# Performance work log

Measured on AMD Instinct MI355X. Metric: run time of the kernel, lower is better.

The kernel has to match this reference:

```python
import jax, jax.numpy as jnp
import numpy as np

INV_SQRT2 = 0.7071067811865476  # 1/sqrt(2), haar dec filter coefficient


def haar_dwt2(x):
    """Single-level 2D Haar DWT matching pywt.dwt2 (even sizes, so 'symmetric'
    padding never contributes). x: [B, H, W] -> (cA, (cH, cV, cD)),
    each [B, H//2, W//2]. pywt haar: cA=(even+odd)/sqrt2, cD=(even-odd)/sqrt2.
    cH = detail along axis0 / approx along axis1 (pywt 'da')."""
    lo = (x[..., ::2] + x[..., 1::2]) * INV_SQRT2   # approx along cols
    hi = (x[..., ::2] - x[..., 1::2]) * INV_SQRT2   # detail along cols
    cA = (lo[..., ::2, :] + lo[..., 1::2, :]) * INV_SQRT2
    cH = (lo[..., ::2, :] - lo[..., 1::2, :]) * INV_SQRT2
    cV = (hi[..., ::2, :] + hi[..., 1::2, :]) * INV_SQRT2
    cD = (hi[..., ::2, :] - hi[..., 1::2, :]) * INV_SQRT2
    return cA, (cH, cV, cD)


def wavedec2_maps(x, levels):
    """pywt.wavedec2 ordering: [cA_L, (cH_L,cV_L,cD_L), ..., (cH_1,cV_1,cD_1)]."""
    a = x
    details = []
    for _ in range(levels):
        a, d = haar_dwt2(a)
        details.append(d)
    maps = [a]
    for d in reversed(details):
        maps.extend(d)
    return maps  # 1 + 3*levels coefficient maps


def setup_inputs() -> dict:
    key = jax.random.key(0)
    k1, k2 = jax.random.split(key)
    B, H, W_img = 64, 1024, 1024
    x = jax.random.normal(k1, (B, 1, H, W_img), dtype=jnp.float32)
    n_maps = 1 + 3 * 2  # levels=2 -> 7
    W = jax.random.normal(k2, (n_maps, 256), dtype=jnp.float32) * (1.0 / np.sqrt(n_maps))
    b = jnp.zeros((256,), dtype=jnp.float32)
    return {"x": x, "W": W, "b": b}


def reference(x, W, b):
    imgs = x[:, 0]                       # [B, H, W]
    B = imgs.shape[0]
    maps = wavedec2_maps(imgs, 2)        # 7 maps of varying spatial size
    # bilinear resize to 8x8, half-pixel centers == torch align_corners=False
    proc = [jax.image.resize(m, (B, 8, 8), method="bilinear") for m in maps]
    feat = jnp.stack(proc, axis=1)       # [B, 7, 8, 8]
    feat = feat.reshape(B, feat.shape[1], 64).transpose(0, 2, 1)  # [B, 64, 7]
    return feat @ W + b                  # [B, 64, 256]
```

## Files before the change

### kernel.cpp

```cpp
#include <hip/hip_runtime.h>
#include <math.h>

#define IS2 0.70710678118654752440f


__device__ __forceinline__ float tri_f(float x) {
    float a = 1.0f - fabsf(x);
    return a > 0.0f ? a : 0.0f;
}

__global__ void init_weights(float* __restrict__ ws) {
    __shared__ float norm512[8];
    __shared__ float norm256[8];
    int t = threadIdx.x;
    if (t < 8) {
        float c = 64.0f * t + 31.5f;
        float s = 0.0f;
        for (int m = 0; m < 512; ++m) s += tri_f((m - c) * (1.0f / 64.0f));
        norm512[t] = s;
    } else if (t < 16) {
        int i = t - 8;
        float c = 32.0f * i + 15.5f;
        float s = 0.0f;
        for (int m = 0; m < 256; ++m) s += tri_f((m - c) * (1.0f / 32.0f));
        norm256[i] = s;
    }
    __syncthreads();

    float* K2 = ws;
    float* K4 = ws + 4096;
    float* Fc = ws + 6144;

    for (int idx = t; idx < 4096; idx += 256) {
        int m2 = idx >> 3, i = idx & 7;
        K2[idx] = IS2 * tri_f((m2 - (64.0f * i + 31.5f)) * (1.0f / 64.0f)) / norm512[i];
    }
    for (int idx = t; idx < 2048; idx += 256) {
        int m4 = idx >> 3, i = idx & 7;
        K4[idx] = 0.5f * tri_f((m4 - (32.0f * i + 15.5f)) * (1.0f / 32.0f)) / norm256[i];
    }
    for (int idx = t; idx < 32768; idx += 256) {
        int jp = idx >> 10, q = idx & 1023;
        int s = jp >> 3, i = jp & 7;
        float v;
        if (s == 0) {
            v = 0.5f * tri_f(((q >> 2) - (32.0f * i + 15.5f)) * (1.0f / 32.0f)) / norm256[i];
        } else if (s == 1) {
            float sg = ((q & 3) < 2) ? 1.0f : -1.0f;
            v = sg * 0.5f * tri_f(((q >> 2) - (32.0f * i + 15.5f)) * (1.0f / 32.0f)) / norm256[i];
        } else if (s == 2) {
            v = IS2 * tri_f(((q >> 1) - (64.0f * i + 31.5f)) * (1.0f / 64.0f)) / norm512[i];
        } else {
            float sg = ((q & 1) == 0) ? 1.0f : -1.0f;
            v = sg * IS2 * tri_f(((q >> 1) - (64.0f * i + 31.5f)) * (1.0f / 64.0f)) / norm512[i];
        }
        Fc[idx] = v;
    }
}

__global__ __launch_bounds__(256) void k1_rowreduce(const float* __restrict__ x,
                                                    const float* __restrict__ ws,
                                                    float* __restrict__ T2) {
    const int b = blockIdx.y;
    const int chunk = blockIdx.x;
    const int t = threadIdx.x;
    const int w = t >> 6;
    const int l = t & 63;
    const int q = chunk * 64 + l;

    const float* K2 = ws;
    const float* K4 = ws + 4096;
    const float* xp = x + (size_t)b * 1048576 + (size_t)(w * 256) * 1024 + q;

    float acc0[8], acc1[8], acc2[8], acc3[8];
#pragma unroll
    for (int i = 0; i < 8; ++i) { acc0[i] = 0.f; acc1[i] = 0.f; acc2[i] = 0.f; acc3[i] = 0.f; }

    const int m2base = w * 128;
    const int m4base = w * 64;

    for (int g = 0; g < 64; ++g) {
        float x0 = xp[0];
        float x1 = xp[1024];
        float x2 = xp[2048];
        float x3 = xp[3072];
        xp += 4096;
        float a2a = x0 + x1, d2a = x0 - x1;
        float a2b = x2 + x3, d2b = x2 - x3;
        float s4 = a2a + a2b, r4 = a2a - a2b;
        const float* wa = K2 + (size_t)(m2base + 2 * g) * 8;
        const float* wb = wa + 8;
        const float* w4 = K4 + (size_t)(m4base + g) * 8;
#pragma unroll
        for (int i = 0; i < 8; ++i) {
            float wai = wa[i], wbi = wb[i], w4i = w4[i];
            acc2[i] += wai * a2a + wbi * a2b;
            acc3[i] += wai * d2a + wbi * d2b;
            acc0[i] += w4i * s4;
            acc1[i] += w4i * r4;
        }
    }

    __shared__ float red[4][32][64];
#pragma unroll
    for (int i = 0; i < 8; ++i) {
        red[w][i][l]      = acc0[i];
        red[w][8 + i][l]  = acc1[i];
        red[w][16 + i][l] = acc2[i];
        red[w][24 + i][l] = acc3[i];
    }
    __syncthreads();

    for (int idx = t; idx < 2048; idx += 256) {
        int jp = idx >> 6, c = idx & 63;
        float s = red[0][jp][c] + red[1][jp][c] + red[2][jp][c] + red[3][jp][c];
        T2[((size_t)b * 32 + jp) * 1024 + chunk * 64 + c] = s;
    }
}

__global__ __launch_bounds__(256) void k2_colreduce(const float* __restrict__ T2,
                                                    const float* __restrict__ Fc,
                                                    float* __restrict__ P) {
    const int b = blockIdx.y;
    const int ch = blockIdx.x;
    const int t = threadIdx.x;

    __shared__ float Tl[32][64];
    __shared__ float Fl[32][65];

    for (int idx = t; idx < 2048; idx += 256) {
        int r = idx >> 6, c = idx & 63;
        Tl[r][c] = T2[((size_t)b * 32 + r) * 1024 + ch * 64 + c];
        Fl[r][c] = Fc[(size_t)r * 1024 + ch * 64 + c];
    }
    __syncthreads();

    const int jpp = t & 31;
    const int jp0 = t >> 5;
    float s0 = 0.f, s1 = 0.f, s2 = 0.f, s3 = 0.f;
#pragma unroll 4
    for (int c = 0; c < 64; ++c) {
        float f = Fl[jpp][c];
        s0 += Tl[jp0][c] * f;
        s1 += Tl[jp0 + 8][c] * f;
        s2 += Tl[jp0 + 16][c] * f;
        s3 += Tl[jp0 + 24][c] * f;
    }
    float* p = P + (((size_t)b * 16 + ch) * 32) * 32 + jpp;
    p[(jp0)      * 32] = s0;
    p[(jp0 + 8)  * 32] = s1;
    p[(jp0 + 16) * 32] = s2;
    p[(jp0 + 24) * 32] = s3;
}

__global__ __launch_bounds__(256) void k3_project(const float* __restrict__ P,
                                                  const float* __restrict__ W,
                                                  const float* __restrict__ bias,
                                                  float* __restrict__ out) {
    const int b = blockIdx.y;
    const int p = blockIdx.x;
    const int n = threadIdx.x;
    const int i = p >> 3, j = p & 7;
    const int rs[7] = {0, 1, 0, 1, 3, 2, 3};
    const int cs[7] = {0, 0, 1, 1, 2, 3, 3};

    float acc = bias[n];
#pragma unroll
    for (int s = 0; s < 7; ++s) {
        const float* pp = P + ((size_t)b * 16 * 32 + rs[s] * 8 + i) * 32 + cs[s] * 8 + j;
        float f = 0.f;
#pragma unroll
        for (int ch = 0; ch < 16; ++ch) f += pp[(size_t)ch * 1024];
        acc += f * W[s * 256 + n];
    }
    out[((size_t)b * 64 + p) * 256 + n] = acc;
}

extern "C" void kernel_launch(void* const* d_in, const int* in_sizes, int n_in,
                              void* d_out, int out_size, void* d_ws, size_t ws_size,
                              hipStream_t stream) {
    (void)in_sizes; (void)n_in; (void)out_size; (void)ws_size;
    const float* x    = (const float*)d_in[0];
    const float* W    = (const float*)d_in[1];
    const float* bias = (const float*)d_in[2];
    float* ws = (float*)d_ws;
    float* Fc = ws + 6144;
    float* T2 = ws + 38912;
    float* P  = ws + 2136064;
    float* out = (float*)d_out;

    hipLaunchKernelGGL(init_weights, dim3(1), dim3(256), 0, stream, ws);
    hipLaunchKernelGGL(k1_rowreduce, dim3(16, 64), dim3(256), 0, stream, x, ws, T2);
    hipLaunchKernelGGL(k2_colreduce, dim3(16, 64), dim3(256), 0, stream, T2, Fc, P);
    hipLaunchKernelGGL(k3_project, dim3(64, 64), dim3(256), 0, stream, P, W, bias, out);
}
```

Baseline: 446.3 us.

## Fuse row and column reductions into one kernel and parallelize weight init

The column-reduction kernel is merged into the row-reduction kernel: partial sums are combined in shared memory and multiplied against a skewed shared copy of the column filter, so the 8 MB T2 intermediate is never written to or read back from global memory and one launch is removed. The weight-init kernel now runs across 152 blocks with closed-form normalisation constants instead of a single block with serial sum loops. In exchange, the fused kernel uses more shared memory (about 40 KB per block), which may lower occupancy.

Result: faster. 412.8 us (-7.5%).

```diff
diff --git a/kernel.cpp b/kernel.cpp
--- a/kernel.cpp
+++ b/kernel.cpp
@@ -9,64 +9,56 @@
     return a > 0.0f ? a : 0.0f;
 }
 
-__global__ void init_weights(float* __restrict__ ws) {
-    __shared__ float norm512[8];
-    __shared__ float norm256[8];
-    int t = threadIdx.x;
-    if (t < 8) {
-        float c = 64.0f * t + 31.5f;
-        float s = 0.0f;
-        for (int m = 0; m < 512; ++m) s += tri_f((m - c) * (1.0f / 64.0f));
-        norm512[t] = s;
-    } else if (t < 16) {
-        int i = t - 8;
-        float c = 32.0f * i + 15.5f;
-        float s = 0.0f;
-        for (int m = 0; m < 256; ++m) s += tri_f((m - c) * (1.0f / 32.0f));
-        norm256[i] = s;
-    }
-    __syncthreads();
+__device__ __forceinline__ float n512f(int i) { return (i == 0 || i == 7) ? 56.0f : 64.0f; }
+__device__ __forceinline__ float n256f(int i) { return (i == 0 || i == 7) ? 28.0f : 32.0f; }
 
-    float* K2 = ws;
-    float* K4 = ws + 4096;
-    float* Fc = ws + 6144;
-
-    for (int idx = t; idx < 4096; idx += 256) {
+__global__ __launch_bounds__(256) void init_weights(float* __restrict__ ws) {
+    int idx = blockIdx.x * 256 + threadIdx.x;
+    if (idx >= 38912) return;
+    if (idx < 4096) {
         int m2 = idx >> 3, i = idx & 7;
-        K2[idx] = IS2 * tri_f((m2 - (64.0f * i + 31.5f)) * (1.0f / 64.0f)) / norm512[i];
-    }
-    for (int idx = t; idx < 2048; idx += 256) {
-        int m4 = idx >> 3, i = idx & 7;
-        K4[idx] = 0.5f * tri_f((m4 - (32.0f * i + 15.5f)) * (1.0f / 32.0f)) / norm256[i];
-    }
-    for (int idx = t; idx < 32768; idx += 256) {
-        int jp = idx >> 10, q = idx & 1023;
+        ws[idx] = IS2 * tri_f((m2 - (64.0f * i + 31.5f)) * (1.0f / 64.0f)) / n512f(i);
+    } else if (idx < 6144) {
+        int j = idx - 4096;
+        int m4 = j >> 3, i = j & 7;
+        ws[idx] = 0.5f * tri_f((m4 - (32.0f * i + 15.5f)) * (1.0f / 32.0f)) / n256f(i);
+    } else {
+        int j = idx - 6144;
+        int jp = j >> 10, q = j & 1023;
         int s = jp >> 3, i = jp & 7;
         float v;
         if (s == 0) {
-            v = 0.5f * tri_f(((q >> 2) - (32.0f * i + 15.5f)) * (1.0f / 32.0f)) / norm256[i];
+            v = 0.5f * tri_f(((q >> 2) - (32.0f * i + 15.5f)) * (1.0f / 32.0f)) / n256f(i);
         } else if (s == 1) {
             float sg = ((q & 3) < 2) ? 1.0f : -1.0f;
-            v = sg * 0.5f * tri_f(((q >> 2) - (32.0f * i + 15.5f)) * (1.0f / 32.0f)) / norm256[i];
+            v = sg * 0.5f * tri_f(((q >> 2) - (32.0f * i + 15.5f)) * (1.0f / 32.0f)) / n256f(i);
         } else if (s == 2) {
-            v = IS2 * tri_f(((q >> 1) - (64.0f * i + 31.5f)) * (1.0f / 64.0f)) / norm512[i];
+            v = IS2 * tri_f(((q >> 1) - (64.0f * i + 31.5f)) * (1.0f / 64.0f)) / n512f(i);
         } else {
             float sg = ((q & 1) == 0) ? 1.0f : -1.0f;
-            v = sg * IS2 * tri_f(((q >> 1) - (64.0f * i + 31.5f)) * (1.0f / 64.0f)) / norm512[i];
+            v = sg * IS2 * tri_f(((q >> 1) - (64.0f * i + 31.5f)) * (1.0f / 64.0f)) / n512f(i);
         }
-        Fc[idx] = v;
+        ws[idx] = v;
     }
 }
 
-__global__ __launch_bounds__(256) void k1_rowreduce(const float* __restrict__ x,
-                                                    const float* __restrict__ ws,
-                                                    float* __restrict__ T2) {
+__global__ __launch_bounds__(256) void k1_fused(const float* __restrict__ x,
+                                                const float* __restrict__ ws,
+                                                float* __restrict__ P) {
     const int b = blockIdx.y;
     const int chunk = blockIdx.x;
     const int t = threadIdx.x;
     const int w = t >> 6;
     const int l = t & 63;
     const int q = chunk * 64 + l;
+
+    __shared__ float red[4][32][64];
+    __shared__ float Fl[2048];
+
+    for (int idx = t; idx < 2048; idx += 256) {
+        int r = idx >> 6, c = idx & 63;
+        Fl[r * 64 + ((c + r) & 63)] = ws[6144 + (size_t)r * 1024 + chunk * 64 + c];
+    }
 
     const float* K2 = ws;
     const float* K4 = ws + 4096;
@@ -101,7 +93,6 @@
         }
     }
 
-    __shared__ float red[4][32][64];
 #pragma unroll
     for (int i = 0; i < 8; ++i) {
         red[w][i][l]      = acc0[i];
@@ -113,25 +104,7 @@
 
     for (int idx = t; idx < 2048; idx += 256) {
         int jp = idx >> 6, c = idx & 63;
-        float s = red[0][jp][c] + red[1][jp][c] + red[2][jp][c] + red[3][jp][c];
-        T2[((size_t)b * 32 + jp) * 1024 + chunk * 64 + c] = s;
-    }
-}
-
-__global__ __launch_bounds__(256) void k2_colreduce(const float* __restrict__ T2,
-                                                    const float* __restrict__ Fc,
-                                                    float* __restrict__ P) {
-    const int b = blockIdx.y;
-    const int ch = blockIdx.x;
-    const int t = threadIdx.x;
-
-    __shared__ float Tl[32][64];
-    __shared__ float Fl[32][65];
-
-    for (int idx = t; idx < 2048; idx += 256) {
-        int r = idx >> 6, c = idx & 63;
-        Tl[r][c] = T2[((size_t)b * 32 + r) * 1024 + ch * 64 + c];
-        Fl[r][c] = Fc[(size_t)r * 1024 + ch * 64 + c];
+        red[0][jp][c] = red[0][jp][c] + red[1][jp][c] + red[2][jp][c] + red[3][jp][c];
     }
     __syncthreads();
 
@@ -140,13 +113,13 @@
     float s0 = 0.f, s1 = 0.f, s2 = 0.f, s3 = 0.f;
 #pragma unroll 4
     for (int c = 0; c < 64; ++c) {
-        float f = Fl[jpp][c];
-        s0 += Tl[jp0][c] * f;
-        s1 += Tl[jp0 + 8][c] * f;
-        s2 += Tl[jp0 + 16][c] * f;
-        s3 += Tl[jp0 + 24][c] * f;
+        float f = Fl[jpp * 64 + ((c + jpp) & 63)];
+        s0 += red[0][jp0][c]      * f;
+        s1 += red[0][jp0 + 8][c]  * f;
+        s2 += red[0][jp0 + 16][c] * f;
+        s3 += red[0][jp0 + 24][c] * f;
     }
-    float* p = P + (((size_t)b * 16 + ch) * 32) * 32 + jpp;
+    float* p = P + (((size_t)b * 16 + chunk) * 32) * 32 + jpp;
     p[(jp0)      * 32] = s0;
     p[(jp0 + 8)  * 32] = s1;
     p[(jp0 + 16) * 32] = s2;
@@ -184,13 +157,10 @@
     const float* W    = (const float*)d_in[1];
     const float* bias = (const float*)d_in[2];
     float* ws = (float*)d_ws;
-    float* Fc = ws + 6144;
-    float* T2 = ws + 38912;
     float* P  = ws + 2136064;
     float* out = (float*)d_out;
 
-    hipLaunchKernelGGL(init_weights, dim3(1), dim3(256), 0, stream, ws);
-    hipLaunchKernelGGL(k1_rowreduce, dim3(16, 64), dim3(256), 0, stream, x, ws, T2);
-    hipLaunchKernelGGL(k2_colreduce, dim3(16, 64), dim3(256), 0, stream, T2, Fc, P);
+    hipLaunchKernelGGL(init_weights, dim3(152), dim3(256), 0, stream, ws);
+    hipLaunchKernelGGL(k1_fused, dim3(16, 64), dim3(256), 0, stream, x, ws, P);
     hipLaunchKernelGGL(k3_project, dim3(64, 64), dim3(256), 0, stream, P, W, bias, out);
 }
```
